# Kernel optimization log

Hardware: AMD Instinct MI355X
Metric: run time of the kernel (lower is better)

## Reference

```python
import jax, jax.numpy as jnp
import numpy as np

N_NODES = 50000
N_EDGES = 800000
EPS = 1e-16

def _gat_layer(x, row, col, W, a_src, a_dst, b, heads, concat):
    N = x.shape[0]
    C = a_src.shape[1]
    h = (x @ W).reshape(N, heads, C)                       # [N,H,C]
    al_src = jnp.sum(h * a_src, axis=-1)                    # [N,H]
    al_dst = jnp.sum(h * a_dst, axis=-1)                    # [N,H]
    e = jax.nn.leaky_relu(al_src[row] + al_dst[col], 0.2)   # [E,H]
    # segment softmax over destination node (col)
    m = jax.ops.segment_max(e, col, num_segments=N)
    e = jnp.exp(e - m[col])
    s = jax.ops.segment_sum(e, col, num_segments=N)
    alpha = e / (s[col] + EPS)                              # [E,H]
    msg = h[row] * alpha[:, :, None]                        # [E,H,C]
    out = jax.ops.segment_sum(msg, col, num_segments=N)     # [N,H,C]
    out = out.reshape(N, heads * C) if concat else out.mean(axis=1)
    return out + b

def setup_inputs() -> dict:
    key = jax.random.key(0)
    ks = jax.random.split(key, 16)
    d_in, hid, d_out, d_edge, H = 64, 64, 32, 16, 4
    inp = {
        "x": jax.random.normal(ks[0], (N_NODES, d_in), jnp.float32),
        "edge_index": jax.random.randint(ks[1], (2, N_EDGES), 0, N_NODES, jnp.int32),
        "edge_attr": jax.random.normal(ks[2], (N_EDGES, d_edge), jnp.float32),
        "W1": jax.random.normal(ks[3], (d_in, H * hid), jnp.float32) * 0.1,
        "a1_src": jax.random.normal(ks[4], (H, hid), jnp.float32) * 0.1,
        "a1_dst": jax.random.normal(ks[5], (H, hid), jnp.float32) * 0.1,
        "b1": jax.random.normal(ks[6], (H * hid,), jnp.float32) * 0.1,
        "W2": jax.random.normal(ks[7], (H * hid, hid), jnp.float32) * 0.05,
        "a2_src": jax.random.normal(ks[8], (1, hid), jnp.float32) * 0.1,
        "a2_dst": jax.random.normal(ks[9], (1, hid), jnp.float32) * 0.1,
        "b2": jax.random.normal(ks[10], (hid,), jnp.float32) * 0.1,
        "Wn": jax.random.normal(ks[11], (hid, d_out), jnp.float32) * 0.1,
        "bn": jax.random.normal(ks[12], (d_out,), jnp.float32) * 0.1,
        "We": jax.random.normal(ks[13], (2 * hid + d_edge, 1), jnp.float32) * 0.1,
        "be": jax.random.normal(ks[14], (1,), jnp.float32) * 0.1,
    }
    return inp

def reference(x, edge_index, edge_attr, W1, a1_src, a1_dst, b1, W2, a2_src, a2_dst, b2, Wn, bn, We, be):
    N = x.shape[0]
    row0, col0 = edge_index[0], edge_index[1]
    # PyG GATConv default: add self loops for message passing
    loops = jnp.arange(N, dtype=edge_index.dtype)
    row = jnp.concatenate([row0, loops])
    col = jnp.concatenate([col0, loops])
    h = jax.nn.elu(_gat_layer(x, row, col, W1, a1_src, a1_dst, b1, heads=4, concat=True))
    h = jax.nn.elu(_gat_layer(h, row, col, W2, a2_src, a2_dst, b2, heads=1, concat=False))
    node_out = h @ Wn + bn                                   # [N, out]
    edge_feat = jnp.concatenate([h[row0], h[col0], edge_attr], axis=1)  # [E, 2*hid+d_edge]
    edge_out = edge_feat @ We + be                           # [E, 1]
    return (node_out, edge_out)
```

## Files before the change

### kernel.cpp

```cpp
#include <hip/hip_runtime.h>
#include <hip/hip_bf16.h>

#define N_NODES 50000
#define N_EDGES 800000
#define N_TOT   850000
#define MAXD    128

#define NBUCK 196
#define BCAP  8192

typedef __hip_bfloat16 bf16;
typedef __attribute__((ext_vector_type(8))) short bf16x8;
typedef __attribute__((ext_vector_type(4))) float f32x4;

__device__ __forceinline__ unsigned short f2bu(float v){
  union { bf16 b; unsigned short u; } cv; cv.b = __float2bfloat16(v); return cv.u;
}
__device__ __forceinline__ float bflo(unsigned int d){ return __uint_as_float(d << 16); }
__device__ __forceinline__ float bfhi(unsigned int d){ return __uint_as_float(d & 0xffff0000u); }

__global__ __launch_bounds__(256) void prep1_kernel(const float* __restrict__ W1, const float* __restrict__ W2,
    const float* __restrict__ a1s, const float* __restrict__ a1d,
    unsigned short* __restrict__ wf1, unsigned short* __restrict__ wf2,
    float* __restrict__ ws1, float* __restrict__ wd1,
    const int* __restrict__ ei, int* __restrict__ bcur, unsigned int* __restrict__ pairbuf){
  __shared__ int hist[NBUCK];
  __shared__ int gbase[NBUCK];
  int b = blockIdx.x, tid = threadIdx.x;
  if (b < 128) {
    int i = b*256 + tid;
    if (i < 16384) {
      int k = i >> 8, n = i & 255;
      int kk = k >> 5, qq = (k >> 3) & 3, j = k & 7, nt = n >> 4, cc = n & 15;
      wf1[(((kk*16 + nt)*4 + qq)*16 + cc)*8 + j] = f2bu(W1[i]);
    } else {
      int i2 = i - 16384;
      int k = i2 >> 6, n = i2 & 63;
      int kk = k >> 5, qq = (k >> 3) & 3, j = k & 7, ch = n >> 4, cc = n & 15;
      wf2[(((kk*4 + ch)*4 + qq)*16 + cc)*8 + j] = f2bu(W2[i2]);
    }
  } else if (b == 128) {
    int k = tid >> 2, h = tid & 3;
    const float* wrow = W1 + k*256 + h*64;
    const float* as = a1s + h*64;
    const float* ad = a1d + h*64;
    float ss = 0.f, sd = 0.f;
    #pragma unroll 8
    for (int c = 0; c < 64; ++c) {
      float wv = wrow[c];
      ss = fmaf(wv, as[c], ss);
      sd = fmaf(wv, ad[c], sd);
    }
    ws1[k*4 + h] = ss;
    wd1[k*4 + h] = sd;
  } else {
    int bb = b - 129;
    if (tid < NBUCK) hist[tid] = 0;
    __syncthreads();
    int base = bb * 4096;
    #pragma unroll 4
    for (int i = 0; i < 16; ++i) {
      int k = base + i*256 + tid;
      if (k < N_TOT) {
        int c = (k < N_EDGES) ? ei[N_EDGES + k] : (k - N_EDGES);
        atomicAdd(&hist[c >> 8], 1);
      }
    }
    __syncthreads();
    if (tid < NBUCK) {
      int h = hist[tid];
      gbase[tid] = h ? (tid*BCAP + atomicAdd(&bcur[tid], h)) : 0;
      hist[tid] = 0;
    }
    __syncthreads();
    #pragma unroll 4
    for (int i = 0; i < 16; ++i) {
      int k = base + i*256 + tid;
      if (k < N_TOT) {
        int r, c;
        if (k < N_EDGES) { r = ei[k]; c = ei[N_EDGES + k]; } else { r = c = k - N_EDGES; }
        int bk = c >> 8;
        int lpos = atomicAdd(&hist[bk], 1);
        pairbuf[gbase[bk] + lpos] = (unsigned)r | ((unsigned)(c & 255) << 16);
      }
    }
  }
}

__global__ __launch_bounds__(256) void prep2_kernel(const unsigned int* __restrict__ pairbuf,
    const int* __restrict__ bcur, int* __restrict__ offs, int* __restrict__ srcs,
    const float* __restrict__ x, const float* __restrict__ ws1, const float* __restrict__ wd1,
    unsigned short* __restrict__ xb, float* __restrict__ al1s, float* __restrict__ al1d){
  __shared__ int sbase[256];
  __shared__ int lhist[256];
  __shared__ int lcur[256];
  __shared__ float sws[64][4], swd[64][4];
  int tid = threadIdx.x;
  if (blockIdx.x < NBUCK) {
    int b = blockIdx.x;
    int sz = 0;
    if (tid < NBUCK) {
      sz = bcur[tid];
      if (sz < 0) sz = 0; if (sz > BCAP) sz = BCAP;
    }
    sbase[tid] = sz;
    lhist[tid] = 0;
    __syncthreads();
    for (int off = 1; off < 256; off <<= 1) {
      int t = (tid >= off) ? sbase[tid - off] : 0;
      __syncthreads();
      sbase[tid] += t;
      __syncthreads();
    }
    int bbase_b = (b == 0) ? 0 : sbase[b - 1];
    int size = sbase[b] - bbase_b;
    int base = b * BCAP;
    for (int j = tid; j < size; j += 256)
      atomicAdd(&lhist[pairbuf[base + j] >> 16], 1);
    __syncthreads();
    int v = lhist[tid];
    lcur[tid] = v;
    __syncthreads();
    for (int off = 1; off < 256; off <<= 1) {
      int t = (tid >= off) ? lcur[tid - off] : 0;
      __syncthreads();
      lcur[tid] += t;
      __syncthreads();
    }
    int excl = lcur[tid] - v;
    int gpos = bbase_b + excl;
    int node = b*256 + tid;
    if (node < N_NODES) offs[node] = gpos;
    if (b == 0 && tid == 0) offs[N_NODES] = N_TOT;
    __syncthreads();
    lcur[tid] = gpos;
    __syncthreads();
    for (int j = tid; j < size; j += 256) {
      unsigned pv = pairbuf[base + j];
      int pos = atomicAdd(&lcur[pv >> 16], 1);
      srcs[pos] = (int)(pv & 0xFFFFu);
    }
  } else {
    sws[tid >> 2][tid & 3] = ws1[tid];
    swd[tid >> 2][tid & 3] = wd1[tid];
    __syncthreads();
    int lane = tid & 63, wave = tid >> 6;
    int g = lane & 15, sub = lane >> 4;
    int n = (blockIdx.x - NBUCK)*16 + wave*4 + sub;
    float4 xv = *(const float4*)(x + (size_t)n*64 + g*4);
    uint2 dd;
    dd.x = (unsigned)f2bu(xv.x) | ((unsigned)f2bu(xv.y) << 16);
    dd.y = (unsigned)f2bu(xv.z) | ((unsigned)f2bu(xv.w) << 16);
    ((uint2*)xb)[(size_t)n*16 + g] = dd;
    int c0 = g*4;
    float ps0 = 0.f, ps1 = 0.f, ps2 = 0.f, ps3 = 0.f;
    float pd0 = 0.f, pd1 = 0.f, pd2 = 0.f, pd3 = 0.f;
    float xc[4] = {xv.x, xv.y, xv.z, xv.w};
    #pragma unroll
    for (int i = 0; i < 4; ++i) {
      int c = c0 + i;
      ps0 = fmaf(xc[i], sws[c][0], ps0); ps1 = fmaf(xc[i], sws[c][1], ps1);
      ps2 = fmaf(xc[i], sws[c][2], ps2); ps3 = fmaf(xc[i], sws[c][3], ps3);
      pd0 = fmaf(xc[i], swd[c][0], pd0); pd1 = fmaf(xc[i], swd[c][1], pd1);
      pd2 = fmaf(xc[i], swd[c][2], pd2); pd3 = fmaf(xc[i], swd[c][3], pd3);
    }
    #pragma unroll
    for (int off = 1; off < 16; off <<= 1) {
      ps0 += __shfl_xor(ps0, off, 64); ps1 += __shfl_xor(ps1, off, 64);
      ps2 += __shfl_xor(ps2, off, 64); ps3 += __shfl_xor(ps3, off, 64);
      pd0 += __shfl_xor(pd0, off, 64); pd1 += __shfl_xor(pd1, off, 64);
      pd2 += __shfl_xor(pd2, off, 64); pd3 += __shfl_xor(pd3, off, 64);
    }
    if (g < 4)      al1s[(size_t)n*4 + g]       = (g==0)?ps0:(g==1)?ps1:(g==2)?ps2:ps3;
    else if (g < 8) al1d[(size_t)n*4 + (g-4)]   = (g==4)?pd0:(g==5)?pd1:(g==6)?pd2:pd3;
  }
}

__global__ __launch_bounds__(256, 8) void attn1x_kernel(const unsigned short* __restrict__ xb,
    const float* __restrict__ al1s, const float* __restrict__ al1d,
    const int* __restrict__ offs, const int* __restrict__ srcs,
    bf16* __restrict__ ag){
  __shared__ __align__(16) float ebuf[4][MAXD+4][4];
  __shared__ int sbuf[4][MAXD+4];

  int wave = threadIdx.x >> 6, lane = threadIdx.x & 63;
  int n = blockIdx.x*4 + wave;
  int start = offs[n], end = offs[n+1];
  int deg = end - start;
  int lim = deg < MAXD ? deg : MAXD;
  float4 aldv = *(const float4*)(al1d + (size_t)n*4);
  float ald0 = aldv.x, ald1 = aldv.y, ald2 = aldv.z, ald3 = aldv.w;

  float s0 = 0.f, s1 = 0.f, s2 = 0.f, s3 = 0.f;
  {
    int idx = lane;
    for (int j = start + lane; j < end; j += 64, idx += 64) {
      int r = srcs[j];
      float4 als = *(const float4*)(al1s + (size_t)r*4);
      float e0 = als.x + ald0; e0 = e0 >= 0.f ? e0 : 0.2f*e0; float p0 = __expf(e0); s0 += p0;
      float e1 = als.y + ald1; e1 = e1 >= 0.f ? e1 : 0.2f*e1; float p1 = __expf(e1); s1 += p1;
      float e2 = als.z + ald2; e2 = e2 >= 0.f ? e2 : 0.2f*e2; float p2 = __expf(e2); s2 += p2;
      float e3 = als.w + ald3; e3 = e3 >= 0.f ? e3 : 0.2f*e3; float p3 = __expf(e3); s3 += p3;
      if (idx < MAXD) {
        sbuf[wave][idx] = r;
        *(float4*)&ebuf[wave][idx][0] = make_float4(p0, p1, p2, p3);
      }
    }
  }
  if (lane < 4) {
    int ip = lim + lane;
    sbuf[wave][ip] = 0;
    *(float4*)&ebuf[wave][ip][0] = make_float4(0.f, 0.f, 0.f, 0.f);
  }
  #pragma unroll
  for (int off = 32; off; off >>= 1) {
    s0 += __shfl_xor(s0, off, 64);
    s1 += __shfl_xor(s1, off, 64);
    s2 += __shfl_xor(s2, off, 64);
    s3 += __shfl_xor(s3, off, 64);
  }
  float inv0 = 1.f/(s0 + 1e-16f), inv1 = 1.f/(s1 + 1e-16f);
  float inv2 = 1.f/(s2 + 1e-16f), inv3 = 1.f/(s3 + 1e-16f);

  int cl = lane & 15, es = lane >> 4;
  float acc[4][4];
  #pragma unroll
  for (int h = 0; h < 4; ++h)
    #pragma unroll
    for (int i = 0; i < 4; ++i) acc[h][i] = 0.f;
  {
    const uint2* base2 = (const uint2*)xb;
    #pragma unroll 2
    for (int jj = 0; jj < lim; jj += 4) {
      int idx = jj + es;
      int r = sbuf[wave][idx];
      float4 pv = *(const float4*)&ebuf[wave][idx][0];
      uint2 d = base2[(size_t)r*16 + cl];
      float c0 = bflo(d.x), c1 = bfhi(d.x), c2 = bflo(d.y), c3 = bfhi(d.y);
      acc[0][0] = fmaf(pv.x, c0, acc[0][0]); acc[0][1] = fmaf(pv.x, c1, acc[0][1]);
      acc[0][2] = fmaf(pv.x, c2, acc[0][2]); acc[0][3] = fmaf(pv.x, c3, acc[0][3]);
      acc[1][0] = fmaf(pv.y, c0, acc[1][0]); acc[1][1] = fmaf(pv.y, c1, acc[1][1]);
      acc[1][2] = fmaf(pv.y, c2, acc[1][2]); acc[1][3] = fmaf(pv.y, c3, acc[1][3]);
      acc[2][0] = fmaf(pv.z, c0, acc[2][0]); acc[2][1] = fmaf(pv.z, c1, acc[2][1]);
      acc[2][2] = fmaf(pv.z, c2, acc[2][2]); acc[2][3] = fmaf(pv.z, c3, acc[2][3]);
      acc[3][0] = fmaf(pv.w, c0, acc[3][0]); acc[3][1] = fmaf(pv.w, c1, acc[3][1]);
      acc[3][2] = fmaf(pv.w, c2, acc[3][2]); acc[3][3] = fmaf(pv.w, c3, acc[3][3]);
    }
  }
  if (deg > MAXD) {
    const uint2* base2 = (const uint2*)xb;
    for (int jj = MAXD; jj < deg; jj += 4) {
      int idx = jj + es;
      bool ok = idx < deg;
      int j = ok ? (start + idx) : start;
      int r = srcs[j];
      float4 als = *(const float4*)(al1s + (size_t)r*4);
      float e0 = als.x + ald0; e0 = e0 >= 0.f ? e0 : 0.2f*e0; float p0 = __expf(e0);
      float e1 = als.y + ald1; e1 = e1 >= 0.f ? e1 : 0.2f*e1; float p1 = __expf(e1);
      float e2 = als.z + ald2; e2 = e2 >= 0.f ? e2 : 0.2f*e2; float p2 = __expf(e2);
      float e3 = als.w + ald3; e3 = e3 >= 0.f ? e3 : 0.2f*e3; float p3 = __expf(e3);
      float m = ok ? 1.f : 0.f;
      uint2 d = base2[(size_t)r*16 + cl];
      float c0 = bflo(d.x)*m, c1 = bfhi(d.x)*m, c2 = bflo(d.y)*m, c3 = bfhi(d.y)*m;
      acc[0][0] = fmaf(p0, c0, acc[0][0]); acc[0][1] = fmaf(p0, c1, acc[0][1]);
      acc[0][2] = fmaf(p0, c2, acc[0][2]); acc[0][3] = fmaf(p0, c3, acc[0][3]);
      acc[1][0] = fmaf(p1, c0, acc[1][0]); acc[1][1] = fmaf(p1, c1, acc[1][1]);
      acc[1][2] = fmaf(p1, c2, acc[1][2]); acc[1][3] = fmaf(p1, c3, acc[1][3]);
      acc[2][0] = fmaf(p2, c0, acc[2][0]); acc[2][1] = fmaf(p2, c1, acc[2][1]);
      acc[2][2] = fmaf(p2, c2, acc[2][2]); acc[2][3] = fmaf(p2, c3, acc[2][3]);
      acc[3][0] = fmaf(p3, c0, acc[3][0]); acc[3][1] = fmaf(p3, c1, acc[3][1]);
      acc[3][2] = fmaf(p3, c2, acc[3][2]); acc[3][3] = fmaf(p3, c3, acc[3][3]);
    }
  }
  #pragma unroll
  for (int h = 0; h < 4; ++h)
    #pragma unroll
    for (int i = 0; i < 4; ++i) {
      acc[h][i] += __shfl_xor(acc[h][i], 16, 64);
      acc[h][i] += __shfl_xor(acc[h][i], 32, 64);
    }
  {
    float invh = (es==0)?inv0:(es==1)?inv1:(es==2)?inv2:inv3;
    float o0 = ((es==0)?acc[0][0]:(es==1)?acc[1][0]:(es==2)?acc[2][0]:acc[3][0]) * invh;
    float o1 = ((es==0)?acc[0][1]:(es==1)?acc[1][1]:(es==2)?acc[2][1]:acc[3][1]) * invh;
    float o2 = ((es==0)?acc[0][2]:(es==1)?acc[1][2]:(es==2)?acc[2][2]:acc[3][2]) * invh;
    float o3 = ((es==0)?acc[0][3]:(es==1)?acc[1][3]:(es==2)?acc[2][3]:acc[3][3]) * invh;
    uint2 dd;
    dd.x = (unsigned)f2bu(o0) | ((unsigned)f2bu(o1) << 16);
    dd.y = (unsigned)f2bu(o2) | ((unsigned)f2bu(o3) << 16);
    ((uint2*)ag)[(size_t)n*64 + lane] = dd;
  }
}

__global__ __launch_bounds__(256) void gemm12_kernel(const unsigned short* __restrict__ ag,
    const unsigned short* __restrict__ wf1, const unsigned short* __restrict__ wf2,
    const float* __restrict__ b1, const float* __restrict__ a2s, const float* __restrict__ a2d,
    bf16* __restrict__ h2pre, float* __restrict__ al2s, float* __restrict__ al2d){
  __shared__ __align__(16) unsigned short ctile[64*264];
  __shared__ __align__(16) float ctile2[64][65];
  int tid = threadIdx.x, wave = tid >> 6, lane = tid & 63;
  int q = lane >> 4, c = lane & 15;
  int n0 = blockIdx.x * 64;

  {
    union { uint4 u; bf16x8 v; } bfr[2][4];
    #pragma unroll
    for (int kk = 0; kk < 2; ++kk)
      #pragma unroll
      for (int nti = 0; nti < 4; ++nti)
        bfr[kk][nti].u = *(const uint4*)(wf1 + (size_t)((((kk*16 + wave*4 + nti)*4 + q)*16 + c)*8));

    float b1v[4];
    #pragma unroll
    for (int nti = 0; nti < 4; ++nti) b1v[nti] = b1[(wave*4 + nti)*16 + c];

    #pragma unroll 1
    for (int st = 0; st < 4; ++st) {
      int row = n0 + st*16 + c;
      if (row >= N_NODES) row = N_NODES - 1;
      bf16x8 afr[2];
      #pragma unroll
      for (int kk = 0; kk < 2; ++kk) {
        union { uint4 u; bf16x8 v; } a;
        a.u = *(const uint4*)(ag + (size_t)row*256 + wave*64 + kk*32 + q*8);
        afr[kk] = a.v;
      }
      #pragma unroll
      for (int nti = 0; nti < 4; ++nti) {
        f32x4 acc = {0.f, 0.f, 0.f, 0.f};
        #pragma unroll
        for (int kk = 0; kk < 2; ++kk)
          acc = __builtin_amdgcn_mfma_f32_16x16x32_bf16(afr[kk], bfr[kk][nti].v, acc, 0, 0, 0);
        int lrow = st*16 + q*4, nt = wave*4 + nti;
        #pragma unroll
        for (int r = 0; r < 4; ++r) {
          float o = acc[r] + b1v[nti];
          o = o > 0.f ? o : expm1f(o);
          ctile[(lrow + r)*264 + nt*16 + c] = f2bu(o);
        }
      }
    }
  }
  __syncthreads();

  {
    union { uint4 u; bf16x8 v; } bfr[8];
    #pragma unroll
    for (int kk = 0; kk < 8; ++kk)
      bfr[kk].u = *(const uint4*)(wf2 + (size_t)((((kk*4 + wave)*4 + q)*16 + c)*8));

    #pragma unroll 1
    for (int st = 0; st < 4; ++st) {
      if (n0 + st*16 >= N_NODES) break;
      f32x4 acc = {0.f, 0.f, 0.f, 0.f};
      int arow = (st*16 + c)*264 + q*8;
      #pragma unroll
      for (int kk = 0; kk < 8; ++kk) {
        union { uint4 u; bf16x8 v; } a;
        a.u = *(const uint4*)&ctile[arow + kk*32];
        acc = __builtin_amdgcn_mfma_f32_16x16x32_bf16(a.v, bfr[kk].v, acc, 0, 0, 0);
      }
      #pragma unroll
      for (int r = 0; r < 4; ++r)
        ctile2[st*16 + q*4 + r][wave*16 + c] = acc[r];
    }
  }
  __syncthreads();

  float as = a2s[lane], ad = a2d[lane];
  #pragma unroll 1
  for (int i = 0; i < 16; ++i) {
    int node = n0 + wave*16 + i;
    if (node >= N_NODES) break;
    float val = ctile2[wave*16 + i][lane];
    ((unsigned short*)h2pre)[(size_t)node*64 + lane] = f2bu(val);
    float ps = val*as, pd = val*ad;
    #pragma unroll
    for (int off = 32; off; off >>= 1) { ps += __shfl_xor(ps, off, 64); pd += __shfl_xor(pd, off, 64); }
    if (lane == 0) { al2s[node] = ps; al2d[node] = pd; }
  }
}

__global__ __launch_bounds__(512, 8) void attn2_kernel(const bf16* __restrict__ h2pre,
    const float* __restrict__ al2s, const float* __restrict__ al2d,
    const int* __restrict__ offs, const int* __restrict__ srcs,
    const float* __restrict__ b2, float* __restrict__ h2f){
  __shared__ float ebuf[8][MAXD+8];
  __shared__ int   sbuf[8][MAXD+8];
  int wave = threadIdx.x >> 6, lane = threadIdx.x & 63;
  int n = blockIdx.x*8 + wave;
  int start = offs[n], end = offs[n+1];
  int deg = end - start;
  int lim = deg < MAXD ? deg : MAXD;
  float ald = al2d[n];

  float sm = 0.f;
  {
    int idx = lane;
    for (int j = start + lane; j < end; j += 64, idx += 64) {
      int r = srcs[j];
      float t = al2s[r] + ald; t = t >= 0.f ? t : 0.2f*t;
      float p = __expf(t); sm += p;
      if (idx < MAXD) { sbuf[wave][idx] = r; ebuf[wave][idx] = p; }
    }
  }
  if (lane < 8) { int ip = lim + lane; sbuf[wave][ip] = 0; ebuf[wave][ip] = 0.f; }
  #pragma unroll
  for (int off = 32; off; off >>= 1) sm += __shfl_xor(sm, off, 64);
  float inv = 1.f/(sm + 1e-16f);

  int cl = lane & 7, es = lane >> 3;
  float acc0 = 0.f, acc1 = 0.f, acc2 = 0.f, acc3 = 0.f;
  float acc4 = 0.f, acc5 = 0.f, acc6 = 0.f, acc7 = 0.f;
  {
    const uint4* base4 = (const uint4*)h2pre;
    #pragma unroll 2
    for (int jj = 0; jj < lim; jj += 8) {
      int idx = jj + es;
      int r = sbuf[wave][idx];
      float p = ebuf[wave][idx];
      uint4 d = base4[(size_t)r*8 + cl];
      acc0 = fmaf(p, bflo(d.x), acc0);
      acc1 = fmaf(p, bfhi(d.x), acc1);
      acc2 = fmaf(p, bflo(d.y), acc2);
      acc3 = fmaf(p, bfhi(d.y), acc3);
      acc4 = fmaf(p, bflo(d.z), acc4);
      acc5 = fmaf(p, bfhi(d.z), acc5);
      acc6 = fmaf(p, bflo(d.w), acc6);
      acc7 = fmaf(p, bfhi(d.w), acc7);
    }
  }
  if (deg > MAXD) {
    const uint4* base4 = (const uint4*)h2pre;
    for (int jj = MAXD; jj < deg; jj += 8) {
      int idx = jj + es;
      bool ok = idx < deg;
      int j = ok ? (start + idx) : start;
      int r = srcs[j];
      float t = al2s[r] + ald; t = t >= 0.f ? t : 0.2f*t;
      float p = ok ? __expf(t) : 0.f;
      uint4 d = base4[(size_t)r*8 + cl];
      acc0 = fmaf(p, bflo(d.x), acc0);
      acc1 = fmaf(p, bfhi(d.x), acc1);
      acc2 = fmaf(p, bflo(d.y), acc2);
      acc3 = fmaf(p, bfhi(d.y), acc3);
      acc4 = fmaf(p, bflo(d.z), acc4);
      acc5 = fmaf(p, bfhi(d.z), acc5);
      acc6 = fmaf(p, bflo(d.w), acc6);
      acc7 = fmaf(p, bfhi(d.w), acc7);
    }
  }
  #pragma unroll
  for (int off = 8; off < 64; off <<= 1) {
    acc0 += __shfl_xor(acc0, off, 64);
    acc1 += __shfl_xor(acc1, off, 64);
    acc2 += __shfl_xor(acc2, off, 64);
    acc3 += __shfl_xor(acc3, off, 64);
    acc4 += __shfl_xor(acc4, off, 64);
    acc5 += __shfl_xor(acc5, off, 64);
    acc6 += __shfl_xor(acc6, off, 64);
    acc7 += __shfl_xor(acc7, off, 64);
  }

  if (es == 0) {
    float4 b2a = *(const float4*)(b2 + cl*8);
    float4 b2b = *(const float4*)(b2 + cl*8 + 4);
    float o0 = acc0*inv + b2a.x; o0 = o0 > 0.f ? o0 : expm1f(o0);
    float o1 = acc1*inv + b2a.y; o1 = o1 > 0.f ? o1 : expm1f(o1);
    float o2 = acc2*inv + b2a.z; o2 = o2 > 0.f ? o2 : expm1f(o2);
    float o3 = acc3*inv + b2a.w; o3 = o3 > 0.f ? o3 : expm1f(o3);
    float o4 = acc4*inv + b2b.x; o4 = o4 > 0.f ? o4 : expm1f(o4);
    float o5 = acc5*inv + b2b.y; o5 = o5 > 0.f ? o5 : expm1f(o5);
    float o6 = acc6*inv + b2b.z; o6 = o6 > 0.f ? o6 : expm1f(o6);
    float o7 = acc7*inv + b2b.w; o7 = o7 > 0.f ? o7 : expm1f(o7);
    *(float4*)(h2f + (size_t)n*64 + cl*8)     = make_float4(o0, o1, o2, o3);
    *(float4*)(h2f + (size_t)n*64 + cl*8 + 4) = make_float4(o4, o5, o6, o7);
  }
}

__global__ __launch_bounds__(256) void head_kernel(const float* __restrict__ h2f,
    const float* __restrict__ Wn, const float* __restrict__ bn, const float* __restrict__ We,
    float* __restrict__ u, float* __restrict__ v, float* __restrict__ node_out){
  __shared__ __align__(16) float sh[8][64];
  int tid = threadIdx.x;
  int nb = blockIdx.x*8;
  {
    float2 t = *(const float2*)(h2f + (size_t)nb*64 + tid*2);
    *(float2*)&sh[tid >> 5][(tid & 31)*2] = t;
  }
  __syncthreads();
  int wave = tid >> 6, lane = tid & 63;
  int sub = lane >> 5, j = lane & 31;
  int local = wave*2 + sub;
  int n = nb + local;
  const float* h = sh[local];
  float a = 0.f;
  #pragma unroll 16
  for (int k = 0; k < 64; ++k)
    a = fmaf(h[k], Wn[k*32 + j], a);
  node_out[(size_t)n*32 + j] = a + bn[j];
  float pu = h[j]*We[j] + h[j+32]*We[j+32];
  float pv = h[j]*We[64+j] + h[j+32]*We[96+j];
  #pragma unroll
  for (int off = 1; off < 32; off <<= 1) {
    pu += __shfl_xor(pu, off, 64);
    pv += __shfl_xor(pv, off, 64);
  }
  if (j == 0) { u[n] = pu; v[n] = pv; }
}

__global__ __launch_bounds__(256) void edge_kernel(const int* __restrict__ ei, const float* __restrict__ ea,
    const float* __restrict__ u, const float* __restrict__ v,
    const float* __restrict__ We, const float* __restrict__ be, float* __restrict__ out){
  int k = blockIdx.x*256 + threadIdx.x;
  int r = ei[k], c = ei[N_EDGES + k];
  float val = u[r] + v[c] + be[0];
  const float4* wp = (const float4*)(We + 128);
  const float4* p  = (const float4*)(ea + (size_t)k*16);
  #pragma unroll
  for (int jj = 0; jj < 4; jj++) {
    float4 q = p[jj], wq = wp[jj];
    val = fmaf(q.x, wq.x, val);
    val = fmaf(q.y, wq.y, val);
    val = fmaf(q.z, wq.z, val);
    val = fmaf(q.w, wq.w, val);
  }
  out[k] = val;
}

extern "C" void kernel_launch(void* const* d_in, const int* in_sizes, int n_in,
                              void* d_out, int out_size, void* d_ws, size_t ws_size,
                              hipStream_t stream) {
  const float* x   = (const float*)d_in[0];
  const int*   ei  = (const int*)d_in[1];
  const float* ea  = (const float*)d_in[2];
  const float* W1  = (const float*)d_in[3];
  const float* a1s = (const float*)d_in[4];
  const float* a1d = (const float*)d_in[5];
  const float* b1  = (const float*)d_in[6];
  const float* W2  = (const float*)d_in[7];
  const float* a2s = (const float*)d_in[8];
  const float* a2d = (const float*)d_in[9];
  const float* b2  = (const float*)d_in[10];
  const float* Wn  = (const float*)d_in[11];
  const float* bn  = (const float*)d_in[12];
  const float* We  = (const float*)d_in[13];
  const float* be  = (const float*)d_in[14];
  float* out = (float*)d_out;

  char* w = (char*)d_ws;
  int*   offs   = (int*)(w);
  unsigned short* wf1 = (unsigned short*)(w + 200016);
  float* ws1    = (float*)(w + 232784);
  float* wd1    = (float*)(w + 233808);
  unsigned short* wf2 = (unsigned short*)(w + 234832);
  int*   bcur   = (int*)(w + 400016);
  int*   srcs   = (int*)(w + 600016);
  float* al1s   = (float*)(w + 4000016);
  float* al1d   = (float*)(w + 4800016);
  float* al2s   = (float*)(w + 5600016);
  float* al2d   = (float*)(w + 5800016);
  float* uu     = (float*)(w + 6000016);
  float* vv     = (float*)(w + 6200016);
  bf16*  h2pre  = (bf16*)(w + 6400016);
  bf16*  ag     = (bf16*)(w + 12800016);
  unsigned int* pairbuf = (unsigned int*)(w + 38400224);
  unsigned short* xb  = (unsigned short*)h2pre;
  float* h2f = (float*)ag;

  hipMemsetAsync(bcur, 0, NBUCK*4, stream);
  prep1_kernel  <<<337, 256, 0, stream>>>(W1, W2, a1s, a1d, wf1, wf2, ws1, wd1, ei, bcur, pairbuf);
  prep2_kernel  <<<NBUCK + N_NODES/16, 256, 0, stream>>>(pairbuf, bcur, offs, srcs,
                                                         x, ws1, wd1, xb, al1s, al1d);
  attn1x_kernel <<<N_NODES/4, 256, 0, stream>>>(xb, al1s, al1d, offs, srcs, ag);
  gemm12_kernel <<<(N_NODES + 63)/64, 256, 0, stream>>>((const unsigned short*)ag, wf1, wf2, b1,
                                                        a2s, a2d, h2pre, al2s, al2d);
  attn2_kernel  <<<N_NODES/8, 512, 0, stream>>>(h2pre, al2s, al2d, offs, srcs, b2, h2f);
  head_kernel   <<<N_NODES/8, 256, 0, stream>>>(h2f, Wn, bn, We, uu, vv, out);
  edge_kernel   <<<N_EDGES/256, 256, 0, stream>>>(ei, ea, uu, vv, We, be, out + (size_t)N_NODES*32);
}
```

Baseline: 287.6 us.

## Compute edge_attr projection in extra blocks of layer-1 attention kernel

The edge_attr·We dot product does not depend on node features, so it moves into extra blocks appended to the attn1x launch and is written to a workspace buffer epart. The final edge kernel then only adds u[r]+v[c]+epart[k]. The aim is to overlap the 51 MB edge_attr read with the gather-bound attention work and shorten the tail kernel. In exchange it writes and rereads a 3.2 MB intermediate, and the extra blocks may compete with attention blocks for bandwidth.

Result: no change. 282.1 us (-1.9%).

```diff
diff --git a/kernel.cpp b/kernel.cpp
--- a/kernel.cpp
+++ b/kernel.cpp
@@ -8,6 +8,8 @@
 
 #define NBUCK 196
 #define BCAP  8192
+#define A1BLK (N_NODES/4)
+#define EPBLK 782
 
 typedef __hip_bfloat16 bf16;
 typedef __attribute__((ext_vector_type(8))) short bf16x8;
@@ -179,9 +181,38 @@
 __global__ __launch_bounds__(256, 8) void attn1x_kernel(const unsigned short* __restrict__ xb,
     const float* __restrict__ al1s, const float* __restrict__ al1d,
     const int* __restrict__ offs, const int* __restrict__ srcs,
-    bf16* __restrict__ ag){
+    bf16* __restrict__ ag,
+    const float* __restrict__ ea, const float* __restrict__ We, const float* __restrict__ be,
+    float* __restrict__ epart){
   __shared__ __align__(16) float ebuf[4][MAXD+4][4];
   __shared__ int sbuf[4][MAXD+4];
+
+  if (blockIdx.x >= A1BLK) {
+    int eb = blockIdx.x - A1BLK;
+    const float4* wp = (const float4*)(We + 128);
+    float4 w0 = wp[0], w1 = wp[1], w2 = wp[2], w3 = wp[3];
+    float bee = be[0];
+    int base = eb*1024 + (int)threadIdx.x;
+    #pragma unroll
+    for (int i = 0; i < 4; ++i) {
+      int k = base + i*256;
+      if (k < N_EDGES) {
+        const float4* p = (const float4*)(ea + (size_t)k*16);
+        float4 q0 = p[0], q1 = p[1], q2 = p[2], q3 = p[3];
+        float val = bee;
+        val = fmaf(q0.x, w0.x, val); val = fmaf(q0.y, w0.y, val);
+        val = fmaf(q0.z, w0.z, val); val = fmaf(q0.w, w0.w, val);
+        val = fmaf(q1.x, w1.x, val); val = fmaf(q1.y, w1.y, val);
+        val = fmaf(q1.z, w1.z, val); val = fmaf(q1.w, w1.w, val);
+        val = fmaf(q2.x, w2.x, val); val = fmaf(q2.y, w2.y, val);
+        val = fmaf(q2.z, w2.z, val); val = fmaf(q2.w, w2.w, val);
+        val = fmaf(q3.x, w3.x, val); val = fmaf(q3.y, w3.y, val);
+        val = fmaf(q3.z, w3.z, val); val = fmaf(q3.w, w3.w, val);
+        epart[k] = val;
+      }
+    }
+    return;
+  }
 
   int wave = threadIdx.x >> 6, lane = threadIdx.x & 63;
   int n = blockIdx.x*4 + wave;
@@ -509,23 +540,12 @@
   if (j == 0) { u[n] = pu; v[n] = pv; }
 }
 
-__global__ __launch_bounds__(256) void edge_kernel(const int* __restrict__ ei, const float* __restrict__ ea,
+__global__ __launch_bounds__(256) void edge_kernel(const int* __restrict__ ei,
     const float* __restrict__ u, const float* __restrict__ v,
-    const float* __restrict__ We, const float* __restrict__ be, float* __restrict__ out){
+    const float* __restrict__ epart, float* __restrict__ out){
   int k = blockIdx.x*256 + threadIdx.x;
   int r = ei[k], c = ei[N_EDGES + k];
-  float val = u[r] + v[c] + be[0];
-  const float4* wp = (const float4*)(We + 128);
-  const float4* p  = (const float4*)(ea + (size_t)k*16);
-  #pragma unroll
-  for (int jj = 0; jj < 4; jj++) {
-    float4 q = p[jj], wq = wp[jj];
-    val = fmaf(q.x, wq.x, val);
-    val = fmaf(q.y, wq.y, val);
-    val = fmaf(q.z, wq.z, val);
-    val = fmaf(q.w, wq.w, val);
-  }
-  out[k] = val;
+  out[k] = u[r] + v[c] + epart[k];
 }
 
 extern "C" void kernel_launch(void* const* d_in, const int* in_sizes, int n_in,
@@ -565,6 +585,7 @@
   bf16*  h2pre  = (bf16*)(w + 6400016);
   bf16*  ag     = (bf16*)(w + 12800016);
   unsigned int* pairbuf = (unsigned int*)(w + 38400224);
+  float* epart  = (float*)(w + 48000000);
   unsigned short* xb  = (unsigned short*)h2pre;
   float* h2f = (float*)ag;
 
@@ -572,10 +593,11 @@
   prep1_kernel  <<<337, 256, 0, stream>>>(W1, W2, a1s, a1d, wf1, wf2, ws1, wd1, ei, bcur, pairbuf);
   prep2_kernel  <<<NBUCK + N_NODES/16, 256, 0, stream>>>(pairbuf, bcur, offs, srcs,
                                                          x, ws1, wd1, xb, al1s, al1d);
-  attn1x_kernel <<<N_NODES/4, 256, 0, stream>>>(xb, al1s, al1d, offs, srcs, ag);
+  attn1x_kernel <<<A1BLK + EPBLK, 256, 0, stream>>>(xb, al1s, al1d, offs, srcs, ag,
+                                                    ea, We, be, epart);
   gemm12_kernel <<<(N_NODES + 63)/64, 256, 0, stream>>>((const unsigned short*)ag, wf1, wf2, b1,
                                                         a2s, a2d, h2pre, al2s, al2d);
   attn2_kernel  <<<N_NODES/8, 512, 0, stream>>>(h2pre, al2s, al2d, offs, srcs, b2, h2f);
   head_kernel   <<<N_NODES/8, 256, 0, stream>>>(h2f, Wn, bn, We, uu, vv, out);
-  edge_kernel   <<<N_EDGES/256, 256, 0, stream>>>(ei, ea, uu, vv, We, be, out + (size_t)N_NODES*32);
-}
+  edge_kernel   <<<N_EDGES/256, 256, 0, stream>>>(ei, uu, vv, epart, out + (size_t)N_NODES*32);
+}
```
